# Kernel tuning notes

Hardware: AMD Instinct MI355X
Metric: run time of the kernel (lower is better)

The kernel has to match this reference:

```python
import jax, jax.numpy as jnp
import numpy as np

B, N, D, H, F = 8, 1024, 1024, 16, 4096
HEAD_DIM = D // H


def layernorm(x, g, b, eps=1e-5):
    m = jnp.mean(x, axis=-1, keepdims=True)
    v = jnp.mean(jnp.square(x - m), axis=-1, keepdims=True)
    return (x - m) * jax.lax.rsqrt(v + eps) * g + b


def setup_inputs() -> dict:
    key = jax.random.key(0)
    ks = jax.random.split(key, 12)
    s = 0.02
    return {
        "src": jax.random.normal(ks[0], (B, N, D), dtype=jnp.float32),
        "mask": jax.random.bernoulli(ks[1], 0.9, (B, N)),  # bool, True = keep token
        "Wqkv": jax.random.normal(ks[2], (3 * D, D), dtype=jnp.float32) * s,
        "Wproj": jax.random.normal(ks[3], (D, D), dtype=jnp.float32) * s,
        "bproj": jnp.zeros((D,), jnp.float32),
        "W1": jax.random.normal(ks[4], (F, D), dtype=jnp.float32) * s,
        "b1": jnp.zeros((F,), jnp.float32),
        "W2": jax.random.normal(ks[5], (D, F), dtype=jnp.float32) * s,
        "b2": jnp.zeros((D,), jnp.float32),
        "g0": jnp.ones((D,), jnp.float32),
        "beta0": jnp.zeros((D,), jnp.float32),
        "g1": jnp.ones((D,), jnp.float32),
        "beta1": jnp.zeros((D,), jnp.float32),
    }


def reference(src, mask, Wqkv, Wproj, bproj, W1, b1, W2, b2, g0, beta0, g1, beta1):
    Bx, Nx, C = src.shape
    # pre-norm + masked self-attention (eval mode: dropouts/drop_path are identity)
    h = layernorm(src, g0, beta0)
    qkv = (h @ Wqkv.T).reshape(Bx, Nx, 3, H, HEAD_DIM).transpose(2, 0, 3, 1, 4)
    q, k, v = qkv[0], qkv[1], qkv[2]  # (B, H, N, head_dim)
    scale = HEAD_DIM ** -0.5
    attn = jnp.einsum('bhnd,bhmd->bhnm', q, k) * scale  # (B, H, N, N)
    pair_mask = (mask[:, None, :] & mask[:, :, None])[:, None, :, :]  # (B,1,N,N)
    neg = -jnp.finfo(attn.dtype).max
    attn = jnp.where(pair_mask, attn, neg)
    attn = jax.nn.softmax(attn, axis=-1)
    a = jnp.einsum('bhnm,bhmd->bhnd', attn, v).transpose(0, 2, 1, 3).reshape(Bx, Nx, C)
    a = a @ Wproj.T + bproj
    x = src + a
    # norm1 + GELU FFN
    x = layernorm(x, g1, beta1)
    ffn = jax.nn.gelu(x @ W1.T + b1, approximate=False) @ W2.T + b2
    return x + ffn
```

## Files before the change

### kernel.cpp

```cpp
#include <hip/hip_runtime.h>
#include <math.h>
#include <stdint.h>
#include <float.h>

#define DEV __device__ __forceinline__

typedef __attribute__((ext_vector_type(8))) short bf16x8;
typedef __attribute__((ext_vector_type(4))) float f32x4;
typedef unsigned short u16;
typedef unsigned int u32;

constexpr int cB = 8, cN = 1024, cD = 1024, cH = 16, cF = 4096, cHD = 64;
constexpr int BH = cB * cH;
constexpr int TOK = cB * cN;

DEV u16 f2bf(float f) {
  u32 x = __float_as_uint(f);
  u32 r = (x + 0x7fffu + ((x >> 16) & 1u)) >> 16;
  return (u16)r;
}

DEV float bf2f(u16 s) { return __uint_as_float(((u32)s) << 16); }

DEV void gl_lds16(const u16* g, u16* l) {
  __builtin_amdgcn_global_load_lds((const __attribute__((address_space(1))) u32*)g,
                                   (__attribute__((address_space(3))) u32*)l, 16, 0, 0);
}

__global__ void mask_norm(const unsigned char* __restrict__ rawb, int* __restrict__ keep) {
  const u32* rawi = (const u32*)rawb;
  const float* rawf = (const float*)rawb;
  int t = threadIdx.x;
  int fb = 0, ff = 0;
  for (int i = t; i < 2048; i += 1024) {
    u32 wv = rawi[i];
    if (wv == 0x3f800000u) ff = 1;
    else if (wv > 1u) fb = 1;
  }
  __shared__ int sf[2];
  if (t == 0) { sf[0] = 0; sf[1] = 0; }
  __syncthreads();
  if (fb) atomicOr(&sf[0], 1);
  if (ff) atomicOr(&sf[1], 1);
  __syncthreads();
  const int isf32 = sf[1];
  const int isbool = sf[0] && !isf32;
  for (int i = t; i < TOK; i += 1024)
    keep[i] = isf32 ? (rawf[i] != 0.f) : (isbool ? (rawb[i] != 0) : (rawi[i] != 0u));
}

__global__ void cvt_k(const float* __restrict__ in, u16* __restrict__ out, int n4) {
  int i = blockIdx.x * blockDim.x + threadIdx.x;
  if (i >= n4) return;
  float4 v = ((const float4*)in)[i];
  short4 o;
  o.x = (short)f2bf(v.x); o.y = (short)f2bf(v.y);
  o.z = (short)f2bf(v.z); o.w = (short)f2bf(v.w);
  ((short4*)out)[i] = o;
}

template <int WF32>
__global__ __launch_bounds__(256) void ln_k(const float* __restrict__ in,
                                            const float* __restrict__ g,
                                            const float* __restrict__ be,
                                            u16* __restrict__ outb,
                                            float* __restrict__ outf) {
  const int row = blockIdx.x;
  const int t = threadIdx.x;
  const float4 v = ((const float4*)(in + (size_t)row * cD))[t];
  float s = v.x + v.y + v.z + v.w;
  float s2 = v.x * v.x + v.y * v.y + v.z * v.z + v.w * v.w;
#pragma unroll
  for (int m = 1; m < 64; m <<= 1) {
    s += __shfl_xor(s, m);
    s2 += __shfl_xor(s2, m);
  }
  __shared__ float ls[8];
  const int w = t >> 6;
  if ((t & 63) == 0) { ls[w] = s; ls[4 + w] = s2; }
  __syncthreads();
  s = ls[0] + ls[1] + ls[2] + ls[3];
  s2 = ls[4] + ls[5] + ls[6] + ls[7];
  const float mean = s * (1.f / cD);
  const float var = fmaxf(s2 * (1.f / cD) - mean * mean, 0.f);
  const float inv = rsqrtf(var + 1e-5f);
  const float4 gg = ((const float4*)g)[t];
  const float4 bb = ((const float4*)be)[t];
  const float o0 = (v.x - mean) * inv * gg.x + bb.x;
  const float o1 = (v.y - mean) * inv * gg.y + bb.y;
  const float o2 = (v.z - mean) * inv * gg.z + bb.z;
  const float o3 = (v.w - mean) * inv * gg.w + bb.w;
  short4 ob;
  ob.x = (short)f2bf(o0); ob.y = (short)f2bf(o1);
  ob.z = (short)f2bf(o2); ob.w = (short)f2bf(o3);
  ((short4*)(outb + (size_t)row * cD))[t] = ob;
  if (WF32) {
    float4 of; of.x = o0; of.y = o1; of.z = o2; of.w = o3;
    ((float4*)(outf + (size_t)row * cD))[t] = of;
  }
}

template <int EP, int BN>
__global__ __launch_bounds__(256) void gemm_bt(const u16* __restrict__ A,
                                               const u16* __restrict__ Bw,
                                               int M, int N, int K, int nbx,
                                               const float* __restrict__ bias,
                                               const float* __restrict__ resid,
                                               float* __restrict__ outf,
                                               u16* __restrict__ ob0,
                                               u16* __restrict__ ob1,
                                               u16* __restrict__ ob2) {
  constexpr int NF = BN / 32;
  constexpr int NBS = BN / 32;
  __shared__ u16 As[128 * 64];
  __shared__ u16 Bs[BN * 64];
  const int t = threadIdx.x;
  const int l = t & 63;
  const int w = t >> 6;
  const int wr = w >> 1, wc = w & 1;
  const int nwg = gridDim.x;
  const int wgid = (blockIdx.x & 7) * (nwg >> 3) + (blockIdx.x >> 3);
  const int bx = wgid % nbx, by = wgid / nbx;
  const int row0 = by * 128;
  const int col0 = bx * BN;

  f32x4 acc[4][NF] = {};

  const int lr = l >> 3, lc = l & 7;
  const int sc = (lc ^ lr) * 8;
  const u16* Ag[4];
  u16* ldsA[4];
#pragma unroll
  for (int i = 0; i < 4; ++i) {
    Ag[i] = A + (size_t)(row0 + i * 32 + w * 8 + lr) * K + sc;
    ldsA[i] = As + i * 2048 + w * 512;
  }
  const u16* Bg[NBS];
  u16* ldsB[NBS];
#pragma unroll
  for (int i = 0; i < NBS; ++i) {
    Bg[i] = Bw + (size_t)(col0 + i * 32 + w * 8 + lr) * K + sc;
    ldsB[i] = Bs + i * 2048 + w * 512;
  }

  const int fr = l & 15, fg = l >> 4;
  const int fx = fr & 7;

  for (int k0 = 0; k0 < K; k0 += 64) {
#pragma unroll
    for (int i = 0; i < 4; ++i) gl_lds16(Ag[i] + k0, ldsA[i]);
#pragma unroll
    for (int i = 0; i < NBS; ++i) gl_lds16(Bg[i] + k0, ldsB[i]);
    __syncthreads();
#pragma unroll
    for (int ks = 0; ks < 2; ++ks) {
      const int xo = ((ks * 4 + fg) ^ fx) * 8;
      bf16x8 af[4], bfr[NF];
#pragma unroll
      for (int m = 0; m < 4; ++m)
        af[m] = *(const bf16x8*)&As[(wr * 64 + m * 16 + fr) * 64 + xo];
#pragma unroll
      for (int n = 0; n < NF; ++n)
        bfr[n] = *(const bf16x8*)&Bs[(wc * (BN / 2) + n * 16 + fr) * 64 + xo];
#pragma unroll
      for (int m = 0; m < 4; ++m)
#pragma unroll
        for (int n = 0; n < NF; ++n)
          acc[m][n] = __builtin_amdgcn_mfma_f32_16x16x32_bf16(af[m], bfr[n], acc[m][n], 0, 0, 0);
    }
    __syncthreads();
  }

#pragma unroll
  for (int m = 0; m < 4; ++m) {
    const int grb = row0 + wr * 64 + m * 16 + (l >> 4) * 4;
#pragma unroll
    for (int n = 0; n < NF; ++n) {
      const int gc = col0 + wc * (BN / 2) + n * 16 + fr;
#pragma unroll
      for (int r = 0; r < 4; ++r) {
        const int gr = grb + r;
        const float cv = acc[m][n][r];
        if constexpr (EP == 0) {
          const int which = gc >> 10;
          const int hh = (gc >> 6) & 15;
          const int dd = gc & 63;
          const int bb = gr >> 10, nn = gr & 1023;
          if (which == 0)
            ob0[(((size_t)bb * cH + hh) * cN + nn) * cHD + dd] = f2bf(cv);
          else if (which == 1)
            ob1[(((size_t)bb * cH + hh) * cN + nn) * cHD + dd] = f2bf(cv);
          else
            ob2[(((size_t)bb * cH + hh) * cHD + dd) * cN + nn] = f2bf(cv);
        } else if constexpr (EP == 1) {
          const size_t idx = (size_t)gr * N + gc;
          outf[idx] = cv + bias[gc] + resid[idx];
        } else if constexpr (EP == 2) {
          const float u = cv + bias[gc];
          const float ge = 0.5f * u * (1.f + erff(u * 0.70710678118654752f));
          ob0[(size_t)gr * N + gc] = f2bf(ge);
        } else {
          const size_t idx = (size_t)gr * N + gc;
          outf[idx] += cv + bias[gc];
        }
      }
    }
  }
}

__global__ __launch_bounds__(256) void attn_k(const u16* __restrict__ Q,
                                              const u16* __restrict__ K,
                                              const u16* __restrict__ Vt,
                                              const int* __restrict__ keep,
                                              u16* __restrict__ out) {
  __shared__ u16 Kbuf[2][32 * 64];
  __shared__ u16 Vbuf[2][64 * 32];
  __shared__ u32 Ps32[4][16 * 20];

  const int t = threadIdx.x, l = t & 63, w = t >> 6;
  const int bh = blockIdx.x, qt = blockIdx.y;
  const int b = bh >> 4, h = bh & 15;
  const u16* Qb = Q + (size_t)bh * cN * cHD;
  const u16* Kb = K + (size_t)bh * cN * cHD;
  const u16* Vb = Vt + (size_t)bh * cHD * cN;
  const int fr = l & 15, fg = l >> 4;
  const int qrow = qt * 64 + w * 16;

  bf16x8 aq0, aq1;
  {
    const bf16x8 q0 = *(const bf16x8*)&Qb[(size_t)(qrow + fr) * cHD + fg * 8];
    const bf16x8 q1 = *(const bf16x8*)&Qb[(size_t)(qrow + fr) * cHD + 32 + fg * 8];
#pragma unroll
    for (int j = 0; j < 8; ++j) {
      aq0[j] = (short)f2bf(bf2f((u16)q0[j]) * 0.125f);
      aq1[j] = (short)f2bf(bf2f((u16)q1[j]) * 0.125f);
    }
  }

  const bool rq = keep[b * cN + qrow + fr] != 0;

  const int p = w * 64 + l;
  const int rK = p >> 3, cK = p & 7;
  const u16* kg = Kb + rK * 64 + ((cK ^ (rK & 7)) * 8);
  const int dV = p >> 2, cV = p & 3;
  const u16* vg = Vb + (size_t)dV * cN + cV * 8;
  u16* ldsK0 = &Kbuf[0][w * 512];
  u16* ldsK1 = &Kbuf[1][w * 512];
  u16* ldsV0 = &Vbuf[0][w * 512];
  u16* ldsV1 = &Vbuf[1][w * 512];

  f32x4 o[4] = {};
  float lpart = 0.f;
  const int kbase = b * cN;
  const int xk0 = (fg ^ (fr & 7)) * 8;
  const int xk1 = ((fg + 4) ^ (fr & 7)) * 8;

  gl_lds16(kg, ldsK0);
  gl_lds16(vg, ldsV0);
  __syncthreads();

  for (int kt = 0; kt < 32; ++kt) {
    const int cur = kt & 1;
    if (kt < 31) {
      gl_lds16(kg + (kt + 1) * 2048, cur ? ldsK0 : ldsK1);
      gl_lds16(vg + (kt + 1) * 32, cur ? ldsV0 : ldsV1);
    }
    const u16* KT = Kbuf[cur];
    const u16* VT = Vbuf[cur];

    float p2[2][4];
#pragma unroll
    for (int n = 0; n < 2; ++n) {
      const int rowoff = (n * 16 + fr) * 64;
      const bf16x8 kA0 = *(const bf16x8*)&KT[rowoff + xk0];
      const bf16x8 kA1 = *(const bf16x8*)&KT[rowoff + xk1];
      f32x4 z = {};
      z = __builtin_amdgcn_mfma_f32_16x16x32_bf16(kA0, aq0, z, 0, 0, 0);
      z = __builtin_amdgcn_mfma_f32_16x16x32_bf16(kA1, aq1, z, 0, 0, 0);
      const int4 kp4 = *(const int4*)&keep[kbase + kt * 32 + n * 16 + fg * 4];
#pragma unroll
      for (int r = 0; r < 4; ++r) {
        const int kpv = (&kp4.x)[r];
        const float pv = rq ? (kpv ? __expf(z[r]) : 0.f) : 1.f;
        p2[n][r] = pv;
        lpart += pv;
      }
    }

#pragma unroll
    for (int n = 0; n < 2; ++n)
#pragma unroll
      for (int rp = 0; rp < 2; ++rp) {
        const u32 dw = (u32)f2bf(p2[n][2 * rp]) | ((u32)f2bf(p2[n][2 * rp + 1]) << 16);
        Ps32[w][fr * 20 + 8 * n + 2 * fg + rp] = dw;
      }
    asm volatile("s_waitcnt lgkmcnt(0)" ::: "memory");
    __builtin_amdgcn_sched_barrier(0);
    const bf16x8 pa = *(const bf16x8*)&Ps32[w][fr * 20 + fg * 4];
#pragma unroll
    for (int n4 = 0; n4 < 4; ++n4) {
      const bf16x8 bv = *(const bf16x8*)&VT[(n4 * 16 + fr) * 32 + fg * 8];
      o[n4] = __builtin_amdgcn_mfma_f32_16x16x32_bf16(pa, bv, o[n4], 0, 0, 0);
    }
    __syncthreads();
  }

  float lsum = lpart;
  lsum += __shfl_xor(lsum, 16);
  lsum += __shfl_xor(lsum, 32);
  float linv[4];
#pragma unroll
  for (int r = 0; r < 4; ++r) linv[r] = 1.f / __shfl(lsum, fg * 4 + r);

#pragma unroll
  for (int n4 = 0; n4 < 4; ++n4) {
#pragma unroll
    for (int r = 0; r < 4; ++r) {
      const int nrow = qrow + fg * 4 + r;
      out[((size_t)b * cN + nrow) * cD + h * 64 + n4 * 16 + fr] = f2bf(o[n4][r] * linv[r]);
    }
  }
}

extern "C" void kernel_launch(void* const* d_in, const int* in_sizes, int n_in,
                              void* d_out, int out_size, void* d_ws, size_t ws_size,
                              hipStream_t stream) {
  (void)in_sizes; (void)n_in; (void)out_size; (void)ws_size;
  const float* src = (const float*)d_in[0];
  const void* maskp = d_in[1];
  const float* Wqkv = (const float*)d_in[2];
  const float* Wproj = (const float*)d_in[3];
  const float* bproj = (const float*)d_in[4];
  const float* W1 = (const float*)d_in[5];
  const float* b1 = (const float*)d_in[6];
  const float* W2 = (const float*)d_in[7];
  const float* b2 = (const float*)d_in[8];
  const float* g0 = (const float*)d_in[9];
  const float* be0 = (const float*)d_in[10];
  const float* g1 = (const float*)d_in[11];
  const float* be1 = (const float*)d_in[12];
  float* out = (float*)d_out;

  char* ws = (char*)d_ws;
  size_t off = 0;
  auto alloc = [&](size_t bytes) -> char* {
    char* p = ws + off;
    off += (bytes + 255) & ~(size_t)255;
    return p;
  };
  u16* wqkv_b = (u16*)alloc((size_t)3 * cD * cD * 2);
  u16* wproj_b = (u16*)alloc((size_t)cD * cD * 2);
  u16* w1_b = (u16*)alloc((size_t)cF * cD * 2);
  u16* w2_b = (u16*)alloc((size_t)cD * cF * 2);
  u16* h_b = (u16*)alloc((size_t)TOK * cD * 2);
  u16* q_b = (u16*)alloc((size_t)TOK * cD * 2);
  u16* k_b = (u16*)alloc((size_t)TOK * cD * 2);
  u16* v_b = (u16*)alloc((size_t)TOK * cD * 2);
  float* x1 = (float*)alloc((size_t)TOK * cD * 4);
  u16* x_b = (u16*)alloc((size_t)TOK * cD * 2);
  u16* f1_b = (u16*)alloc((size_t)TOK * cF * 2);
  int* keep = (int*)alloc((size_t)TOK * 4);

  mask_norm<<<1, 1024, 0, stream>>>((const unsigned char*)maskp, keep);
  cvt_k<<<(3 * cD * cD / 4 + 255) / 256, 256, 0, stream>>>(Wqkv, wqkv_b, 3 * cD * cD / 4);
  cvt_k<<<(cD * cD / 4 + 255) / 256, 256, 0, stream>>>(Wproj, wproj_b, cD * cD / 4);
  cvt_k<<<(cF * cD / 4 + 255) / 256, 256, 0, stream>>>(W1, w1_b, cF * cD / 4);
  cvt_k<<<(cD * cF / 4 + 255) / 256, 256, 0, stream>>>(W2, w2_b, cD * cF / 4);
  ln_k<0><<<TOK, 256, 0, stream>>>(src, g0, be0, h_b, nullptr);

  {
    const int nbx = 3 * cD / 128;
    gemm_bt<0, 128><<<nbx * (TOK / 128), 256, 0, stream>>>(
        h_b, wqkv_b, TOK, 3 * cD, cD, nbx, nullptr, nullptr, nullptr, q_b, k_b, v_b);
  }
  attn_k<<<dim3(BH, cN / 64), 256, 0, stream>>>(q_b, k_b, v_b, keep, h_b);
  {
    const int nbx = cD / 64;
    gemm_bt<1, 64><<<nbx * (TOK / 128), 256, 0, stream>>>(
        h_b, wproj_b, TOK, cD, cD, nbx, bproj, src, x1, nullptr, nullptr, nullptr);
  }
  ln_k<1><<<TOK, 256, 0, stream>>>(x1, g1, be1, x_b, out);
  {
    const int nbx = cF / 128;
    gemm_bt<2, 128><<<nbx * (TOK / 128), 256, 0, stream>>>(
        x_b, w1_b, TOK, cF, cD, nbx, b1, nullptr, nullptr, f1_b, nullptr, nullptr);
  }
  {
    const int nbx = cD / 64;
    gemm_bt<3, 64><<<nbx * (TOK / 128), 256, 0, stream>>>(
        f1_b, w2_b, TOK, cD, cF, nbx, b2, nullptr, out, nullptr, nullptr, nullptr);
  }
}
```

Before: 580.0 us.

## Double-buffer GEMM LDS tiles with direct global-to-LDS prefetch two stages ahead

The GEMM kernel now keeps two LDS buffers for the A and B tiles. It issues the global-to-LDS loads for the next k-tile while the MFMAs run on the current one, using explicit vmcnt waits and barriers in place of the previous load-sync-compute-sync loop. The goal is to hide global memory latency behind matrix math. The cost is double the LDS footprint, which may reduce occupancy, and the hand-tuned vmcnt counts must match the number of loads issued per stage.

```diff
diff --git a/kernel.cpp b/kernel.cpp
--- a/kernel.cpp
+++ b/kernel.cpp
@@ -112,8 +112,8 @@
                                                u16* __restrict__ ob2) {
   constexpr int NF = BN / 32;
   constexpr int NBS = BN / 32;
-  __shared__ u16 As[128 * 64];
-  __shared__ u16 Bs[BN * 64];
+  __shared__ u16 As[2][128 * 64];
+  __shared__ u16 Bs[2][BN * 64];
   const int t = threadIdx.x;
   const int l = t & 63;
   const int w = t >> 6;
@@ -129,47 +129,78 @@
   const int lr = l >> 3, lc = l & 7;
   const int sc = (lc ^ lr) * 8;
   const u16* Ag[4];
-  u16* ldsA[4];
+  int ldsAo[4];
 #pragma unroll
   for (int i = 0; i < 4; ++i) {
     Ag[i] = A + (size_t)(row0 + i * 32 + w * 8 + lr) * K + sc;
-    ldsA[i] = As + i * 2048 + w * 512;
+    ldsAo[i] = i * 2048 + w * 512;
   }
   const u16* Bg[NBS];
-  u16* ldsB[NBS];
+  int ldsBo[NBS];
 #pragma unroll
   for (int i = 0; i < NBS; ++i) {
     Bg[i] = Bw + (size_t)(col0 + i * 32 + w * 8 + lr) * K + sc;
-    ldsB[i] = Bs + i * 2048 + w * 512;
+    ldsBo[i] = i * 2048 + w * 512;
   }
 
   const int fr = l & 15, fg = l >> 4;
   const int fx = fr & 7;
-
-  for (int k0 = 0; k0 < K; k0 += 64) {
-#pragma unroll
-    for (int i = 0; i < 4; ++i) gl_lds16(Ag[i] + k0, ldsA[i]);
-#pragma unroll
-    for (int i = 0; i < NBS; ++i) gl_lds16(Bg[i] + k0, ldsB[i]);
-    __syncthreads();
+  const int nt = K >> 6;
+
+  auto STAGE = [&](int tile, int buf) {
+    const int k0 = tile * 64;
+#pragma unroll
+    for (int i = 0; i < 4; ++i) gl_lds16(Ag[i] + k0, &As[buf][ldsAo[i]]);
+#pragma unroll
+    for (int i = 0; i < NBS; ++i) gl_lds16(Bg[i] + k0, &Bs[buf][ldsBo[i]]);
+  };
+  auto COMPUTE = [&](int buf) {
 #pragma unroll
     for (int ks = 0; ks < 2; ++ks) {
       const int xo = ((ks * 4 + fg) ^ fx) * 8;
       bf16x8 af[4], bfr[NF];
 #pragma unroll
       for (int m = 0; m < 4; ++m)
-        af[m] = *(const bf16x8*)&As[(wr * 64 + m * 16 + fr) * 64 + xo];
+        af[m] = *(const bf16x8*)&As[buf][(wr * 64 + m * 16 + fr) * 64 + xo];
 #pragma unroll
       for (int n = 0; n < NF; ++n)
-        bfr[n] = *(const bf16x8*)&Bs[(wc * (BN / 2) + n * 16 + fr) * 64 + xo];
+        bfr[n] = *(const bf16x8*)&Bs[buf][(wc * (BN / 2) + n * 16 + fr) * 64 + xo];
 #pragma unroll
       for (int m = 0; m < 4; ++m)
 #pragma unroll
         for (int n = 0; n < NF; ++n)
           acc[m][n] = __builtin_amdgcn_mfma_f32_16x16x32_bf16(af[m], bfr[n], acc[m][n], 0, 0, 0);
     }
-    __syncthreads();
-  }
+  };
+#define WAIT_NL()                                                   \
+  do {                                                              \
+    if constexpr (BN == 128)                                        \
+      asm volatile("s_waitcnt vmcnt(8)" ::: "memory");              \
+    else                                                            \
+      asm volatile("s_waitcnt vmcnt(6)" ::: "memory");              \
+    __builtin_amdgcn_sched_barrier(0);                              \
+  } while (0)
+
+  STAGE(0, 0);
+  STAGE(1, 1);
+  WAIT_NL();
+  __builtin_amdgcn_s_barrier();
+
+  for (int tt = 0; tt < nt - 2; ++tt) {
+    const int cur = tt & 1;
+    COMPUTE(cur);
+    __builtin_amdgcn_sched_barrier(0);
+    __builtin_amdgcn_s_barrier();
+    STAGE(tt + 2, cur);
+    WAIT_NL();
+    __builtin_amdgcn_s_barrier();
+  }
+  COMPUTE((nt - 2) & 1);
+  asm volatile("s_waitcnt vmcnt(0)" ::: "memory");
+  __builtin_amdgcn_sched_barrier(0);
+  __builtin_amdgcn_s_barrier();
+  COMPUTE((nt - 1) & 1);
+#undef WAIT_NL
 
 #pragma unroll
   for (int m = 0; m < 4; ++m) {
```

Result: slower. 642.6 us (+10.8%).
